# Kernel optimization log

Hardware: AMD Instinct MI355X
Metric: run time of the kernel (lower is better)

The kernel has to match this reference:

```python
import jax, jax.numpy as jnp
import numpy as np

N_NODES = 50000
N_EDGES = 1600000
D = 128
MU = 1.0
EPS = 1e-06


def setup_inputs() -> dict:
    key = jax.random.key(0)
    ks = jax.random.split(key, 6)
    x = jax.random.normal(ks[0], (N_NODES, D), dtype=jnp.float32)
    edge_index = jax.random.randint(ks[1], (2, N_EDGES), 0, N_NODES, dtype=jnp.int64)
    edge_weight = jax.random.uniform(ks[2], (N_EDGES,), dtype=jnp.float32)
    s = 1.0 / np.sqrt(D)  # nn.Linear-style init scale
    W_chi = jax.random.uniform(ks[3], (D, D), dtype=jnp.float32, minval=-s, maxval=s)
    W_phi = jax.random.uniform(ks[4], (D, D), dtype=jnp.float32, minval=-s, maxval=s)
    W_varphi = jax.random.uniform(ks[5], (D, D), dtype=jnp.float32, minval=-s, maxval=s)
    return {"x": x, "edge_index": edge_index, "edge_weight": edge_weight,
            "W_chi": W_chi, "W_phi": W_phi, "W_varphi": W_varphi}


def reference(x, edge_index, edge_weight, W_chi, W_phi, W_varphi):
    num_nodes = x.shape[0]
    row, col = edge_index[0], edge_index[1]

    # degree_i = sum of edge weights over outgoing edges (scatter_add by row)
    degree = jax.ops.segment_sum(edge_weight, row, num_segments=num_nodes)

    # Phi_chi: per-node tanh of L2 norm of Theta_chi(x)
    Phi_chi = jnp.tanh(jnp.linalg.norm(x @ W_chi.T, axis=1))  # [N]

    x_row = x[row]            # [E, D] gather
    x_col = x[col]            # [E, D] gather

    # Theta_phi(Theta_chi(.)) on gathered endpoints
    x_src = (x_row @ W_chi.T) @ W_phi.T   # [E, D]
    x_dst = (x_col @ W_chi.T) @ W_phi.T   # [E, D]
    Phi_phi = jnp.tanh(jnp.abs(jnp.sum(x_src * x_dst, axis=1)))  # [E]

    diff = x_row - x_col                  # [E, D]
    Phi_varphi = jnp.tanh(1.0 / (jnp.linalg.norm(diff @ W_varphi.T, axis=1) + EPS))  # [E]

    Phi = edge_weight / degree[row] * Phi_phi * Phi_varphi / Phi_chi[row]  # [E]

    energies = Phi[:, None] * diff        # [E, D]
    x_star = jax.ops.segment_sum(energies, row, num_segments=num_nodes)  # [N, D]

    return x - (1.0 / MU) * x_star
```

## Files before the change

kernel.cpp:

```cpp
#include <hip/hip_runtime.h>
#include <hip/hip_bf16.h>

#define NNODES 50000
#define NEDGES 1600000
#define DD 128
#define EPSF 1e-6f
#define NB_SCAN 196

using u32 = unsigned int;
using u16 = unsigned short;
using u64 = unsigned long long;
typedef __attribute__((ext_vector_type(8))) short v8s;
typedef __attribute__((ext_vector_type(4))) float v4f;
typedef __attribute__((ext_vector_type(4))) int   v4i;
typedef __attribute__((ext_vector_type(2))) float v2f;

static __device__ __forceinline__ float b2f16(u16 v) { return __uint_as_float(((u32)v) << 16); }
static __device__ __forceinline__ u16 f2b(float f) {
    u32 u = __float_as_uint(f);
    return (u16)((u + 0x7fffu + ((u >> 16) & 1u)) >> 16);
}
static __device__ __forceinline__ float tanh_pos(float a) {
    float e = __expf(-2.f * a);
    return __fdividef(1.f - e, 1.f + e);
}

#define OFF_GFRAG  0
#define OFF_PHICHI 98304
#define OFF_VSX    298304
#define OFF_CNT    698304
#define OFF_START  898304
#define OFF_BSUM   1098320
#define OFF_BOFF   1099120
#define OFF_ABSC   1099920
#define OFF_AQ     1499920
#define OFF_BQ     7899920
#define OFF_XB     14299920
#define OFF_XQ     27099920
#define OFF_EREC   33499920
#define OFF_WCOMB  33499920
#define OFF_RANK   39899920
#define WS_NEED_RANK 43099920ull

static __device__ __forceinline__ void gstore(u16* gf, int mat, int a, int c, float v) {
    int lane = (((a >> 3) & 3) << 4) | (c & 15);
    int u = ((((mat*8 + (c >> 4))*4 + (a >> 5))*64 + lane) << 3) | (a & 7);
    gf[u] = f2b(v);
}

#define HB (NEDGES/256)
#define XBLK (NNODES/4)

template<bool RANK>
__global__ __launch_bounds__(256) void k_prep(const int* __restrict__ ei,
                                              const float* __restrict__ x,
                                              u32* __restrict__ cnt,
                                              u16* __restrict__ xb,
                                              char* __restrict__ xq,
                                              float* __restrict__ vsx,
                                              u16* __restrict__ rank) {
    int b = blockIdx.x, t = threadIdx.x;
    if (b < HB) {
        int e = b*256 + t;
        if (RANK) rank[e] = (u16)atomicAdd(&cnt[ei[e]], 1u);
        else      atomicAdd(&cnt[ei[e]], 1u);
        return;
    }
    int w = t >> 6, lane = t & 63;
    int node = (b - HB)*4 + w;
    float2 xv = ((const float2*)(x + (size_t)node*DD))[lane];
    u32 pk = (u32)f2b(xv.x) | ((u32)f2b(xv.y) << 16);
    ((u32*)xb)[node*64 + lane] = pk;
    float m = fmaxf(fabsf(xv.x), fabsf(xv.y));
    #pragma unroll
    for (int mask = 1; mask < 64; mask <<= 1)
        m = fmaxf(m, __shfl_xor(m, mask));
    float inv = (m > 0.f) ? 127.f/m : 0.f;
    int q0 = (int)rintf(xv.x*inv), q1 = (int)rintf(xv.y*inv);
    ((u16*)xq)[node*64 + lane] = (u16)((q0 & 0xff) | ((q1 & 0xff) << 8));
    if (lane == 0) vsx[2*node + 1] = m * (1.f/127.f);
}

__global__ __launch_bounds__(256) void k_w1(const float* __restrict__ Wchi,
                                            const float* __restrict__ Wphi,
                                            const float* __restrict__ Wvphi,
                                            float* __restrict__ wcomb,
                                            u16* __restrict__ gf) {
    int b = blockIdx.x, t = threadIdx.x;
    if (b < 64) {
        int idx = b*256 + t;
        int i = idx >> 7, k = idx & 127;
        float acc = 0.f;
        #pragma unroll 8
        for (int m = 0; m < DD; ++m)
            acc = fmaf(Wphi[i*DD+m], Wchi[m*DD+k], acc);
        wcomb[i*DD+k] = acc;
    } else {
        const float* W = (b < 128) ? Wvphi : Wchi;
        int mat = (b < 128) ? 1 : 2;
        int idx = ((b & 63))*256 + t;
        int a = idx >> 7, c = idx & 127;
        float acc = 0.f;
        #pragma unroll 8
        for (int m = 0; m < DD; ++m)
            acc = fmaf(W[m*DD+a], W[m*DD+c], acc);
        gstore(gf, mat, a, c, acc);
    }
}

__global__ __launch_bounds__(256) void k_scan_bsum(const u32* __restrict__ cnt,
                                                   u32* __restrict__ bsum,
                                                   const float* __restrict__ wcomb,
                                                   u16* __restrict__ gf) {
    if (blockIdx.x >= NB_SCAN) {
        int idx = (blockIdx.x - NB_SCAN)*256 + threadIdx.x;
        int a = idx >> 7, c = idx & 127;
        float acc = 0.f;
        #pragma unroll 8
        for (int m = 0; m < DD; ++m)
            acc = fmaf(wcomb[m*DD+a], wcomb[m*DD+c], acc);
        gstore(gf, 0, a, c, acc);
        return;
    }
    __shared__ u32 s[256];
    int i = blockIdx.x*256 + threadIdx.x;
    s[threadIdx.x] = (i < NNODES) ? cnt[i] : 0u;
    __syncthreads();
    for (int off = 128; off > 0; off >>= 1) {
        if (threadIdx.x < off) s[threadIdx.x] += s[threadIdx.x + off];
        __syncthreads();
    }
    if (threadIdx.x == 0) bsum[blockIdx.x] = s[0];
}

__global__ __launch_bounds__(256) void k_scan_boff(const u32* __restrict__ bsum,
                                                   u32* __restrict__ boff) {
    __shared__ u32 s[256];
    int t = threadIdx.x;
    u32 v = (t < NB_SCAN) ? bsum[t] : 0u;
    s[t] = v;
    __syncthreads();
    for (int off = 1; off < 256; off <<= 1) {
        u32 a = (t >= off) ? s[t - off] : 0u;
        __syncthreads();
        s[t] += a;
        __syncthreads();
    }
    if (t < NB_SCAN) boff[t] = s[t] - v;
}

__global__ __launch_bounds__(256) void k_scan_final(const u32* __restrict__ cnt,
                                                    const u32* __restrict__ boff,
                                                    u32* __restrict__ start,
                                                    u32* __restrict__ cursor) {
    __shared__ u32 s[256];
    int t = threadIdx.x;
    int i = blockIdx.x*256 + t;
    u32 v = (i < NNODES) ? cnt[i] : 0u;
    s[t] = v;
    __syncthreads();
    for (int off = 1; off < 256; off <<= 1) {
        u32 a = (t >= off) ? s[t - off] : 0u;
        __syncthreads();
        s[t] += a;
        __syncthreads();
    }
    if (i < NNODES) {
        u32 val = boff[blockIdx.x] + (s[t] - v);
        start[i]  = val;
        cursor[i] = val;
        if (i == NNODES-1) start[NNODES] = val + v;
    }
}

#define SB (NEDGES/256)
#define GB 782

template<bool RANK>
__global__ __launch_bounds__(256) void k_mid(const int* __restrict__ ei,
                                             const float* __restrict__ ew,
                                             const u32* __restrict__ start,
                                             u32* __restrict__ cursor,
                                             const u16* __restrict__ rank,
                                             u32* __restrict__ erec,
                                             const u16* __restrict__ xb,
                                             float* __restrict__ ws,
                                             char* __restrict__ aq,
                                             char* __restrict__ bq,
                                             float* __restrict__ absc) {
    int b = blockIdx.x, t = threadIdx.x;
    if (b % 9 != 0) {
        int eb = b - b/9 - 1;
        int e = eb*256 + t;
        int r = __builtin_nontemporal_load(&ei[e]);
        u32 pos;
        if (RANK) pos = start[r] + (u32)__builtin_nontemporal_load(&rank[e]);
        else      pos = atomicAdd(&cursor[r], 1u);
        u32 c  = (u32)__builtin_nontemporal_load(&ei[NEDGES + e]);
        u32 wb = (u32)f2b(__builtin_nontemporal_load(&ew[e])) & 0x7fffu;
        erec[pos] = (c << 15) | wb;
        return;
    }
    __shared__ u16 xs[4][16][DD];
    int w = t >> 6, l = t & 63;
    int l15 = l & 15, lq = l >> 4;
    int nb = (b/9)*64 + w*16;
    if (nb >= NNODES) return;

    const v8s* xbv = (const v8s*)(xb + (size_t)(nb + l15)*DD);
    v8s af[4];
    #pragma unroll
    for (int kk = 0; kk < 4; ++kk) {
        af[kk] = xbv[kk*4 + lq];
        *(v8s*)&xs[w][l15][kk*32 + lq*8] = af[kk];
    }
    const v8s* gf = (const v8s*)ws;
    float* phichi = ws + OFF_PHICHI/4;
    float* vsx    = ws + OFF_VSX/4;
    float sa4[4] = {0.f, 0.f, 0.f, 0.f};

    #pragma unroll
    for (int mat = 0; mat < 3; ++mat) {
        v4f acc[8];
        #pragma unroll
        for (int nt = 0; nt < 8; ++nt) acc[nt] = (v4f){0.f,0.f,0.f,0.f};
        #pragma unroll
        for (int kk = 0; kk < 4; ++kk)
            #pragma unroll
            for (int nt = 0; nt < 8; ++nt)
                acc[nt] = __builtin_amdgcn_mfma_f32_16x16x32_bf16(
                    af[kk], gf[((mat*8 + nt)*4 + kk)*64 + l], acc[nt], 0, 0, 0);
        if (mat < 2) {
            float mx[4] = {0.f, 0.f, 0.f, 0.f};
            #pragma unroll
            for (int nt = 0; nt < 8; ++nt)
                #pragma unroll
                for (int r = 0; r < 4; ++r)
                    mx[r] = fmaxf(mx[r], fabsf(acc[nt][r]));
            #pragma unroll
            for (int mask = 1; mask < 16; mask <<= 1)
                #pragma unroll
                for (int r = 0; r < 4; ++r)
                    mx[r] = fmaxf(mx[r], __shfl_xor(mx[r], mask));
            float iv[4], sc[4];
            #pragma unroll
            for (int r = 0; r < 4; ++r) {
                iv[r] = (mx[r] > 0.f) ? 127.f/mx[r] : 0.f;
                sc[r] = mx[r] * (1.f/127.f);
            }
            char* qdst = mat ? bq : aq;
            #pragma unroll
            for (int nt = 0; nt < 8; ++nt)
                #pragma unroll
                for (int r = 0; r < 4; ++r)
                    qdst[(size_t)(nb + lq*4 + r)*128 + nt*16 + l15] =
                        (char)(int)rintf(acc[nt][r]*iv[r]);
            if (mat == 0) {
                #pragma unroll
                for (int r = 0; r < 4; ++r) sa4[r] = sc[r];
            } else if (l15 == 0) {
                #pragma unroll
                for (int r = 0; r < 4; ++r)
                    *(v2f*)&absc[2*(nb + lq*4 + r)] = (v2f){sa4[r], sc[r]};
            }
        }
        if (mat >= 1) {
            float p0 = 0.f, p1 = 0.f, p2 = 0.f, p3 = 0.f;
            #pragma unroll
            for (int nt = 0; nt < 8; ++nt) {
                int nn = nt*16 + l15;
                p0 = fmaf(b2f16(xs[w][lq*4+0][nn]), acc[nt][0], p0);
                p1 = fmaf(b2f16(xs[w][lq*4+1][nn]), acc[nt][1], p1);
                p2 = fmaf(b2f16(xs[w][lq*4+2][nn]), acc[nt][2], p2);
                p3 = fmaf(b2f16(xs[w][lq*4+3][nn]), acc[nt][3], p3);
            }
            #pragma unroll
            for (int mask = 1; mask < 16; mask <<= 1) {
                p0 += __shfl_xor(p0, mask);
                p1 += __shfl_xor(p1, mask);
                p2 += __shfl_xor(p2, mask);
                p3 += __shfl_xor(p3, mask);
            }
            if (l15 == 0) {
                int n0 = nb + lq*4;
                if (mat == 1) {
                    vsx[2*(n0+0)] = p0; vsx[2*(n0+1)] = p1;
                    vsx[2*(n0+2)] = p2; vsx[2*(n0+3)] = p3;
                } else {
                    phichi[n0+0] = tanh_pos(sqrtf(fmaxf(p0, 0.f)));
                    phichi[n0+1] = tanh_pos(sqrtf(fmaxf(p1, 0.f)));
                    phichi[n0+2] = tanh_pos(sqrtf(fmaxf(p2, 0.f)));
                    phichi[n0+3] = tanh_pos(sqrtf(fmaxf(p3, 0.f)));
                }
            }
        }
    }
}

__global__ __launch_bounds__(256) void k_accum(const float* __restrict__ x,
                                               const float* __restrict__ phichi,
                                               const float* __restrict__ vsx,
                                               const float* __restrict__ absc,
                                               const u32* __restrict__ start,
                                               const u32* __restrict__ erec,
                                               const char* __restrict__ xq,
                                               const char* __restrict__ aq,
                                               const char* __restrict__ bq,
                                               float* __restrict__ out) {
    __shared__ float red[4][8][132];
    int w = threadIdx.x >> 6, lane = threadIdx.x & 63;
    int node = blockIdx.x*4 + w;
    int l15 = lane & 15, lq = lane >> 4;

    u32 s0 = start[node];
    u32 n  = start[node+1] - s0;
    float vq_r = vsx[2*node];
    float2 sab = *(const float2*)&absc[2*node];

    v4i zero4 = {0, 0, 0, 0};
    v4i afr[2];
    {
        const char* src = (l15 == 1) ? bq : aq;
        const v4i* p = (const v4i*)(src + (size_t)node*128);
        bool keep = (l15 < 2);
        #pragma unroll
        for (int kk = 0; kk < 2; ++kk) {
            v4i v = p[kk*4 + lq];
            afr[kk] = keep ? v : zero4;
        }
    }

    float accl[2][16];
    #pragma unroll
    for (int kk = 0; kk < 2; ++kk)
        #pragma unroll
        for (int j = 0; j < 16; ++j) accl[kk][j] = 0.f;
    float sphi = 0.f, wsum = 0.f;

    u32 ntiles = (n + 15) >> 4;

    auto ldr = [&](u32 tt) -> u32 {
        u32 off = tt*16 + (u32)l15;
        u32 eidx = (off < n) ? (s0 + off) : s0;
        return __builtin_nontemporal_load(&erec[eidx]);
    };

    if (ntiles) {
        u32 rc = ldr(0);
        for (u32 tt = 0; tt < ntiles; ++tt) {
            u32 rn = (tt + 1 < ntiles) ? ldr(tt + 1) : rc;
            u32 c = rc >> 15;
            bool valid = (tt*16 + (u32)l15) < n;
            float w_e = valid ? __uint_as_float((rc & 0x7fffu) << 16) : 0.f;
            float2 vx = *(const float2*)&vsx[2*c];
            const v4i* xcv = (const v4i*)(xq + (size_t)c*128);
            v4i bfr[2];
            bfr[0] = xcv[lq];
            bfr[1] = xcv[4 + lq];

            v4i d = zero4;
            d = __builtin_amdgcn_mfma_i32_16x16x64_i8(afr[0], bfr[0], d, 0, 0, 0);
            d = __builtin_amdgcn_mfma_i32_16x16x64_i8(afr[1], bfr[1], d, 0, 0, 0);
            float adot = (float)d[0] * (sab.x * vx.y);
            float bdot = (float)d[1] * (sab.y * vx.y);
            float ss = fmaxf(vq_r + vx.x - 2.f*bdot, 0.f);
            float psi = w_e * tanh_pos(fabsf(adot)) * tanh_pos(__fdividef(1.f, sqrtf(ss) + EPSF));
            float psi_b = __shfl(psi, l15);
            sphi += psi_b;
            wsum += w_e;
            float psx = psi_b * vx.y;
            #pragma unroll
            for (int kk = 0; kk < 2; ++kk) {
                const int* pw = (const int*)&bfr[kk];
                #pragma unroll
                for (int wd = 0; wd < 4; ++wd) {
                    int word = pw[wd];
                    accl[kk][wd*4+0] = fmaf(psx, (float)((word << 24) >> 24), accl[kk][wd*4+0]);
                    accl[kk][wd*4+1] = fmaf(psx, (float)((word << 16) >> 24), accl[kk][wd*4+1]);
                    accl[kk][wd*4+2] = fmaf(psx, (float)((word <<  8) >> 24), accl[kk][wd*4+2]);
                    accl[kk][wd*4+3] = fmaf(psx, (float)( word        >> 24), accl[kk][wd*4+3]);
                }
            }
            rc = rn;
        }
    }

    #pragma unroll
    for (int mask = 1; mask < 16; mask <<= 1) {
        sphi += __shfl_xor(sphi, mask);
        wsum += __shfl_xor(wsum, mask);
    }

    #pragma unroll
    for (int kk = 0; kk < 2; ++kk)
        #pragma unroll
        for (int j = 0; j < 16; ++j)
            accl[kk][j] += __shfl_xor(accl[kk][j], 1);

    if ((l15 & 1) == 0) {
        int e8 = l15 >> 1;
        #pragma unroll
        for (int kk = 0; kk < 2; ++kk) {
            int base = kk*64 + lq*16;
            *(float4*)&red[w][e8][base]      = *(float4*)&accl[kk][0];
            *(float4*)&red[w][e8][base + 4]  = *(float4*)&accl[kk][4];
            *(float4*)&red[w][e8][base + 8]  = *(float4*)&accl[kk][8];
            *(float4*)&red[w][e8][base + 12] = *(float4*)&accl[kk][12];
        }
    }
    __syncthreads();
    float a0 = 0.f, a1 = 0.f;
    #pragma unroll
    for (int e = 0; e < 8; ++e) {
        float2 v = *(const float2*)&red[w][e][lane*2];
        a0 += v.x; a1 += v.y;
    }

    float ia = (n == 0) ? 0.f : __fdividef(1.f, wsum * phichi[node]);
    float scale = 1.f - ia * sphi;
    float2 xv = *(const float2*)(x + (size_t)node*DD + lane*2);
    v2f o;
    o.x = xv.x*scale + ia*a0;
    o.y = xv.y*scale + ia*a1;
    __builtin_nontemporal_store(o, (v2f*)(out + (size_t)node*DD + lane*2));
}

extern "C" void kernel_launch(void* const* d_in, const int* in_sizes, int n_in,
                              void* d_out, int out_size, void* d_ws, size_t ws_size,
                              hipStream_t stream) {
    const float* x     = (const float*)d_in[0];
    const int*   ei    = (const int*)d_in[1];
    const float* ew    = (const float*)d_in[2];
    const float* Wchi  = (const float*)d_in[3];
    const float* Wphi  = (const float*)d_in[4];
    const float* Wvphi = (const float*)d_in[5];
    float* out = (float*)d_out;
    float* ws  = (float*)d_ws;
    char*  wsb = (char*)d_ws;

    float* phichi = (float*)(wsb + OFF_PHICHI);
    float* vsx    = (float*)(wsb + OFF_VSX);
    u32*   cnt    = (u32*)  (wsb + OFF_CNT);
    u32*   cursor = (u32*)  (wsb + OFF_CNT);
    u32*   start  = (u32*)  (wsb + OFF_START);
    u32*   bsum   = (u32*)  (wsb + OFF_BSUM);
    u32*   boff   = (u32*)  (wsb + OFF_BOFF);
    u16*   gf     = (u16*)  (wsb + OFF_GFRAG);
    float* absc   = (float*)(wsb + OFF_ABSC);
    char*  aq     = (char*) (wsb + OFF_AQ);
    char*  bq     = (char*) (wsb + OFF_BQ);
    u16*   xb     = (u16*)  (wsb + OFF_XB);
    char*  xq     = (char*) (wsb + OFF_XQ);
    u32*   erec   = (u32*)  (wsb + OFF_EREC);
    float* wcomb  = (float*)(wsb + OFF_WCOMB);
    u16*   rank   = (u16*)  (wsb + OFF_RANK);

    bool use_rank = (ws_size >= (size_t)WS_NEED_RANK);

    hipMemsetAsync(wsb + OFF_CNT, 0, 200000, stream);
    if (use_rank) {
        k_prep<true><<<dim3(HB+XBLK), dim3(256), 0, stream>>>(ei, x, cnt, xb, xq, vsx, rank);
    } else {
        k_prep<false><<<dim3(HB+XBLK), dim3(256), 0, stream>>>(ei, x, cnt, xb, xq, vsx, rank);
    }
    k_w1<<<dim3(192), dim3(256), 0, stream>>>(Wchi, Wphi, Wvphi, wcomb, gf);
    k_scan_bsum<<<dim3(NB_SCAN+64), dim3(256), 0, stream>>>(cnt, bsum, wcomb, gf);
    k_scan_boff<<<dim3(1), dim3(256), 0, stream>>>(bsum, boff);
    k_scan_final<<<dim3(NB_SCAN), dim3(256), 0, stream>>>(cnt, boff, start, cursor);
    if (use_rank) {
        k_mid<true><<<dim3(SB+GB), dim3(256), 0, stream>>>(ei, ew, start, cursor, rank, erec, xb, ws, aq, bq, absc);
    } else {
        k_mid<false><<<dim3(SB+GB), dim3(256), 0, stream>>>(ei, ew, start, cursor, rank, erec, xb, ws, aq, bq, absc);
    }
    k_accum<<<dim3(NNODES/4), dim3(256), 0, stream>>>(x, phichi, vsx, absc, start, erec, xq, aq, bq, out);
}
```

Baseline: 231.5 us.

## Replace global atomic row histogram with partitioned LDS histograms and prefix offsets

The row-degree count and per-edge rank are now built by a partitioned histogram: 64 edge partitions by 4 row ranges, each counting in LDS atomics and writing per-partition counts. A rowsum kernel then turns these counts into per-partition exclusive offsets plus total counts, and the scatter pass adds the partition base to the local rank. The aim is to remove 1.6M contended global atomics. The weight-precompute kernel is merged into k_prep to save a launch. The cost is a larger workspace (12.8MB of partition bases), each edge index being read four times by the histogram blocks, and a serial 64-step loop per row in k_rowsum.

```diff
diff --git a/kernel.cpp b/kernel.cpp
--- a/kernel.cpp
+++ b/kernel.cpp
@@ -6,6 +6,9 @@
 #define DD 128
 #define EPSF 1e-6f
 #define NB_SCAN 196
+#define NPART 64
+#define EPP 25000
+#define RGSZ 12500
 
 using u32 = unsigned int;
 using u16 = unsigned short;
@@ -40,7 +43,8 @@
 #define OFF_EREC   33499920
 #define OFF_WCOMB  33499920
 #define OFF_RANK   39899920
-#define WS_NEED_RANK 43099920ull
+#define OFF_CBASE  43099920
+#define WS_NEED_RANK 55899920ull
 
 static __device__ __forceinline__ void gstore(u16* gf, int mat, int a, int c, float v) {
     int lane = (((a >> 3) & 3) << 4) | (c & 15);
@@ -51,44 +55,82 @@
 #define HB (NEDGES/256)
 #define XBLK (NNODES/4)
 
+__global__ __launch_bounds__(256) void k_hist(const int* __restrict__ ei,
+                                              u16* __restrict__ rank,
+                                              u32* __restrict__ cbase) {
+    __shared__ u32 lcnt[RGSZ];
+    int p = blockIdx.x >> 2, rg = blockIdx.x & 3;
+    int t = threadIdx.x;
+    for (int i = t; i < RGSZ; i += 256) lcnt[i] = 0;
+    __syncthreads();
+    int base = rg * RGSZ;
+    for (int i = t; i < EPP; i += 256) {
+        int e = p*EPP + i;
+        int r = ei[e];
+        u32 rr = (u32)(r - base);
+        if (rr < RGSZ) {
+            u32 old = atomicAdd(&lcnt[rr], 1u);
+            rank[e] = (u16)old;
+        }
+    }
+    __syncthreads();
+    u32* dst = cbase + (size_t)p*NNODES + base;
+    for (int i = t; i < RGSZ; i += 256) dst[i] = lcnt[i];
+}
+
+__global__ __launch_bounds__(256) void k_rowsum(u32* __restrict__ cbase,
+                                                u32* __restrict__ cnt) {
+    int r = blockIdx.x*256 + threadIdx.x;
+    if (r >= NNODES) return;
+    u32 running = 0;
+    #pragma unroll
+    for (int p = 0; p < NPART; ++p) {
+        u32 c = cbase[(size_t)p*NNODES + r];
+        cbase[(size_t)p*NNODES + r] = running;
+        running += c;
+    }
+    cnt[r] = running;
+}
+
 template<bool RANK>
 __global__ __launch_bounds__(256) void k_prep(const int* __restrict__ ei,
                                               const float* __restrict__ x,
+                                              const float* __restrict__ Wchi,
+                                              const float* __restrict__ Wphi,
+                                              const float* __restrict__ Wvphi,
                                               u32* __restrict__ cnt,
                                               u16* __restrict__ xb,
                                               char* __restrict__ xq,
                                               float* __restrict__ vsx,
-                                              u16* __restrict__ rank) {
+                                              float* __restrict__ wcomb,
+                                              u16* __restrict__ gf) {
     int b = blockIdx.x, t = threadIdx.x;
-    if (b < HB) {
-        int e = b*256 + t;
-        if (RANK) rank[e] = (u16)atomicAdd(&cnt[ei[e]], 1u);
-        else      atomicAdd(&cnt[ei[e]], 1u);
+    if (!RANK) {
+        if (b < HB) {
+            atomicAdd(&cnt[ei[b*256 + t]], 1u);
+            return;
+        }
+        b -= HB;
+    }
+    if (b < XBLK) {
+        int w = t >> 6, lane = t & 63;
+        int node = b*4 + w;
+        float2 xv = ((const float2*)(x + (size_t)node*DD))[lane];
+        u32 pk = (u32)f2b(xv.x) | ((u32)f2b(xv.y) << 16);
+        ((u32*)xb)[node*64 + lane] = pk;
+        float m = fmaxf(fabsf(xv.x), fabsf(xv.y));
+        #pragma unroll
+        for (int mask = 1; mask < 64; mask <<= 1)
+            m = fmaxf(m, __shfl_xor(m, mask));
+        float inv = (m > 0.f) ? 127.f/m : 0.f;
+        int q0 = (int)rintf(xv.x*inv), q1 = (int)rintf(xv.y*inv);
+        ((u16*)xq)[node*64 + lane] = (u16)((q0 & 0xff) | ((q1 & 0xff) << 8));
+        if (lane == 0) vsx[2*node + 1] = m * (1.f/127.f);
         return;
     }
-    int w = t >> 6, lane = t & 63;
-    int node = (b - HB)*4 + w;
-    float2 xv = ((const float2*)(x + (size_t)node*DD))[lane];
-    u32 pk = (u32)f2b(xv.x) | ((u32)f2b(xv.y) << 16);
-    ((u32*)xb)[node*64 + lane] = pk;
-    float m = fmaxf(fabsf(xv.x), fabsf(xv.y));
-    #pragma unroll
-    for (int mask = 1; mask < 64; mask <<= 1)
-        m = fmaxf(m, __shfl_xor(m, mask));
-    float inv = (m > 0.f) ? 127.f/m : 0.f;
-    int q0 = (int)rintf(xv.x*inv), q1 = (int)rintf(xv.y*inv);
-    ((u16*)xq)[node*64 + lane] = (u16)((q0 & 0xff) | ((q1 & 0xff) << 8));
-    if (lane == 0) vsx[2*node + 1] = m * (1.f/127.f);
-}
-
-__global__ __launch_bounds__(256) void k_w1(const float* __restrict__ Wchi,
-                                            const float* __restrict__ Wphi,
-                                            const float* __restrict__ Wvphi,
-                                            float* __restrict__ wcomb,
-                                            u16* __restrict__ gf) {
-    int b = blockIdx.x, t = threadIdx.x;
-    if (b < 64) {
-        int idx = b*256 + t;
+    int bb = b - XBLK;
+    if (bb < 64) {
+        int idx = bb*256 + t;
         int i = idx >> 7, k = idx & 127;
         float acc = 0.f;
         #pragma unroll 8
@@ -96,9 +138,9 @@
             acc = fmaf(Wphi[i*DD+m], Wchi[m*DD+k], acc);
         wcomb[i*DD+k] = acc;
     } else {
-        const float* W = (b < 128) ? Wvphi : Wchi;
-        int mat = (b < 128) ? 1 : 2;
-        int idx = ((b & 63))*256 + t;
+        const float* W = (bb < 128) ? Wvphi : Wchi;
+        int mat = (bb < 128) ? 1 : 2;
+        int idx = ((bb & 63))*256 + t;
         int a = idx >> 7, c = idx & 127;
         float acc = 0.f;
         #pragma unroll 8
@@ -182,6 +224,7 @@
                                              const u32* __restrict__ start,
                                              u32* __restrict__ cursor,
                                              const u16* __restrict__ rank,
+                                             const u32* __restrict__ cbase,
                                              u32* __restrict__ erec,
                                              const u16* __restrict__ xb,
                                              float* __restrict__ ws,
@@ -194,8 +237,13 @@
         int e = eb*256 + t;
         int r = __builtin_nontemporal_load(&ei[e]);
         u32 pos;
-        if (RANK) pos = start[r] + (u32)__builtin_nontemporal_load(&rank[e]);
-        else      pos = atomicAdd(&cursor[r], 1u);
+        if (RANK) {
+            int p = e / EPP;
+            pos = start[r] + cbase[(size_t)p*NNODES + r]
+                + (u32)__builtin_nontemporal_load(&rank[e]);
+        } else {
+            pos = atomicAdd(&cursor[r], 1u);
+        }
         u32 c  = (u32)__builtin_nontemporal_load(&ei[NEDGES + e]);
         u32 wb = (u32)f2b(__builtin_nontemporal_load(&ew[e])) & 0x7fffu;
         erec[pos] = (c << 15) | wb;
@@ -454,23 +502,31 @@
     u32*   erec   = (u32*)  (wsb + OFF_EREC);
     float* wcomb  = (float*)(wsb + OFF_WCOMB);
     u16*   rank   = (u16*)  (wsb + OFF_RANK);
+    u32*   cbase  = (u32*)  (wsb + OFF_CBASE);
 
     bool use_rank = (ws_size >= (size_t)WS_NEED_RANK);
 
-    hipMemsetAsync(wsb + OFF_CNT, 0, 200000, stream);
     if (use_rank) {
-        k_prep<true><<<dim3(HB+XBLK), dim3(256), 0, stream>>>(ei, x, cnt, xb, xq, vsx, rank);
+        k_hist<<<dim3(256), dim3(256), 0, stream>>>(ei, rank, cbase);
+        k_prep<true><<<dim3(XBLK+192), dim3(256), 0, stream>>>(ei, x, Wchi, Wphi, Wvphi,
+                                                               cnt, xb, xq, vsx, wcomb, gf);
+        k_rowsum<<<dim3(NB_SCAN), dim3(256), 0, stream>>>(cbase, cnt);
     } else {
-        k_prep<false><<<dim3(HB+XBLK), dim3(256), 0, stream>>>(ei, x, cnt, xb, xq, vsx, rank);
-    }
-    k_w1<<<dim3(192), dim3(256), 0, stream>>>(Wchi, Wphi, Wvphi, wcomb, gf);
+        hipError_t err = hipMemsetAsync(wsb + OFF_CNT, 0, 200000, stream);
+        (void)err;
+        k_prep<false><<<dim3(HB+XBLK+192), dim3(256), 0, stream>>>(ei, x, Wchi, Wphi, Wvphi,
+                                                                   cnt, xb, xq, vsx, wcomb, gf);
+    }
     k_scan_bsum<<<dim3(NB_SCAN+64), dim3(256), 0, stream>>>(cnt, bsum, wcomb, gf);
     k_scan_boff<<<dim3(1), dim3(256), 0, stream>>>(bsum, boff);
     k_scan_final<<<dim3(NB_SCAN), dim3(256), 0, stream>>>(cnt, boff, start, cursor);
     if (use_rank) {
-        k_mid<true><<<dim3(SB+GB), dim3(256), 0, stream>>>(ei, ew, start, cursor, rank, erec, xb, ws, aq, bq, absc);
+        k_mid<true><<<dim3(SB+GB), dim3(256), 0, stream>>>(ei, ew, start, cursor, rank, cbase,
+                                                           erec, xb, ws, aq, bq, absc);
     } else {
-        k_mid<false><<<dim3(SB+GB), dim3(256), 0, stream>>>(ei, ew, start, cursor, rank, erec, xb, ws, aq, bq, absc);
-    }
-    k_accum<<<dim3(NNODES/4), dim3(256), 0, stream>>>(x, phichi, vsx, absc, start, erec, xq, aq, bq, out);
-}
+        k_mid<false><<<dim3(SB+GB), dim3(256), 0, stream>>>(ei, ew, start, cursor, rank, cbase,
+                                                            erec, xb, ws, aq, bq, absc);
+    }
+    k_accum<<<dim3(NNODES/4), dim3(256), 0, stream>>>(x, phichi, vsx, absc, start, erec,
+                                                      xq, aq, bq, out);
+}
```

After: 226.3 us. -2.2%, faster.
